# Performance work log

Measured on AMD Instinct MI355X. Metric: run time of the kernel, lower is better.

## Reference

```python
import jax, jax.numpy as jnp
import numpy as np
import math

D = 2048
NH = 16
HD = D // NH
MULT = 4
EPS = 1e-6


def rmsnorm(x, g):
    norm = jax.lax.rsqrt(jnp.mean(x * x, axis=-1, keepdims=True) + EPS)
    return g * x * norm


def setup_inputs() -> dict:
    key = jax.random.key(0)
    ks = jax.random.split(key, 8)
    s = 0.02  # keep activations in a sane range
    return {
        "x": jax.random.normal(ks[0], (2, 2048, D), dtype=jnp.float32),
        "g1": jnp.ones((D,), dtype=jnp.float32),
        "wq": jax.random.normal(ks[1], (D, D), dtype=jnp.float32) * s,
        "wk": jax.random.normal(ks[2], (D, D), dtype=jnp.float32) * s,
        "wv": jax.random.normal(ks[3], (D, D), dtype=jnp.float32) * s,
        "wo": jax.random.normal(ks[4], (D, D), dtype=jnp.float32) * s,
        "g2": jnp.ones((D,), dtype=jnp.float32),
        "w_up": jax.random.normal(ks[5], (2 * D * MULT, D), dtype=jnp.float32) * s,
        "w_down": jax.random.normal(ks[6], (D, D * MULT), dtype=jnp.float32) * s,
    }


def reference(x, g1, wq, wk, wv, wo, g2, w_up, w_down):
    B, T, _ = x.shape
    # --- causal self-attention with pre-RMSNorm ---
    h = rmsnorm(x, g1)
    q = (h @ wq.T).reshape(B, T, NH, HD).transpose(0, 2, 1, 3)  # [B,H,T,hd]
    k = (h @ wk.T).reshape(B, T, NH, HD).transpose(0, 2, 1, 3)
    v = (h @ wv.T).reshape(B, T, NH, HD).transpose(0, 2, 1, 3)
    att = jnp.einsum("bhtd,bhsd->bhts", q, k) / math.sqrt(HD)  # [B,H,T,T]
    neg = jnp.finfo(att.dtype).min
    causal = jnp.triu(jnp.full((T, T), neg, dtype=att.dtype), k=1)
    att = att + causal
    w = jax.nn.softmax(att, axis=-1)
    z = jnp.einsum("bhts,bhsd->bhtd", w, v)  # [B,H,T,hd]
    z = z.transpose(0, 2, 1, 3).reshape(B, T, D)
    x = x + z @ wo.T
    # --- SwiGLU-style FFN (GELU gate) with pre-RMSNorm ---
    h2 = rmsnorm(x, g2)
    uv = h2 @ w_up.T  # [B,T,2*D*MULT]
    u, vgate = jnp.split(uv, 2, axis=-1)
    ff = (jax.nn.gelu(u, approximate=False) * vgate) @ w_down.T
    return x + ff
```

## Files before the change

### kernel.cpp

```cpp
#include <hip/hip_runtime.h>
#include <math.h>

typedef __bf16 bf16_t;
typedef __bf16 bf16x8 __attribute__((ext_vector_type(8)));
typedef __bf16 bf16x4 __attribute__((ext_vector_type(4)));
typedef float f32x4 __attribute__((ext_vector_type(4)));

#define D_MODEL 2048
#define N_HEADS 16
#define HEAD_D 128
#define SEQ 2048
#define NTOK 4096
#define DFF 8192
#define UPN 16384

#define GLDS16(g, l) __builtin_amdgcn_global_load_lds( \
    (const __attribute__((address_space(1))) void*)(g), \
    (__attribute__((address_space(3))) void*)(l), 16, 0, 0)

__global__ __launch_bounds__(256) void cvt_bf16_kernel(const float* __restrict__ in,
                                                       bf16_t* __restrict__ out, long n4) {
    long i = (long)blockIdx.x * 256 + threadIdx.x;
    long stride = (long)gridDim.x * 256;
    for (; i < n4; i += stride) {
        float4 f = ((const float4*)in)[i];
        bf16x4 v;
        v[0] = (bf16_t)f.x; v[1] = (bf16_t)f.y; v[2] = (bf16_t)f.z; v[3] = (bf16_t)f.w;
        ((bf16x4*)out)[i] = v;
    }
}

__global__ __launch_bounds__(256) void rmsnorm_kernel(const float* __restrict__ x,
                                                      const float* __restrict__ g,
                                                      bf16_t* __restrict__ out) {
    int row = blockIdx.x;
    const float* xr = x + (size_t)row * D_MODEL;
    int c0 = threadIdx.x * 8;
    float4 a = *(const float4*)&xr[c0];
    float4 b = *(const float4*)&xr[c0 + 4];
    float ss = a.x*a.x + a.y*a.y + a.z*a.z + a.w*a.w
             + b.x*b.x + b.y*b.y + b.z*b.z + b.w*b.w;
    #pragma unroll
    for (int off = 1; off < 64; off <<= 1) ss += __shfl_xor(ss, off);
    __shared__ float red[4];
    if ((threadIdx.x & 63) == 0) red[threadIdx.x >> 6] = ss;
    __syncthreads();
    float norm = rsqrtf((red[0] + red[1] + red[2] + red[3]) * (1.f / D_MODEL) + 1e-6f);
    float4 ga = *(const float4*)&g[c0];
    float4 gb = *(const float4*)&g[c0 + 4];
    bf16x8 o;
    o[0] = (bf16_t)(a.x * ga.x * norm); o[1] = (bf16_t)(a.y * ga.y * norm);
    o[2] = (bf16_t)(a.z * ga.z * norm); o[3] = (bf16_t)(a.w * ga.w * norm);
    o[4] = (bf16_t)(b.x * gb.x * norm); o[5] = (bf16_t)(b.y * gb.y * norm);
    o[6] = (bf16_t)(b.z * gb.z * norm); o[7] = (bf16_t)(b.w * gb.w * norm);
    *(bf16x8*)&out[(size_t)row * D_MODEL + c0] = o;
}

template<int EPI>
__global__ __launch_bounds__(256)
void gemm_bt(const bf16_t* __restrict__ A, const bf16_t* __restrict__ W,
             void* __restrict__ outp, const float* __restrict__ res,
             int M, int N, int K, float alpha)
{
    __shared__ __align__(16) bf16_t As[128 * 32];
    __shared__ __align__(16) bf16_t Bs[128 * 32];
    const int tid = threadIdx.x;
    const int m0 = blockIdx.y * 128, n0 = blockIdx.x * 128;
    const int wave = tid >> 6, lane = tid & 63;
    const int wr = wave >> 1, wc = wave & 1;
    const int lr = lane & 15, lg = lane >> 4;
    const int srow = (lane >> 2), scol = (lane & 3) * 8;
    f32x4 acc[4][4] = {};
    for (int k0 = 0; k0 < K; k0 += 32) {
        __syncthreads();
        #pragma unroll
        for (int t = 0; t < 2; ++t) {
            int rbase = wave * 32 + t * 16;
            int r = rbase + srow;
            GLDS16(&A[(size_t)(m0 + r) * K + k0 + scol], &As[rbase * 32]);
            GLDS16(&W[(size_t)(n0 + r) * K + k0 + scol], &Bs[rbase * 32]);
        }
        __syncthreads();
        bf16x8 af[4], bfr[4];
        #pragma unroll
        for (int m = 0; m < 4; ++m) af[m] = *(const bf16x8*)&As[(wr * 64 + m * 16 + lr) * 32 + lg * 8];
        #pragma unroll
        for (int n = 0; n < 4; ++n) bfr[n] = *(const bf16x8*)&Bs[(wc * 64 + n * 16 + lr) * 32 + lg * 8];
        #pragma unroll
        for (int m = 0; m < 4; ++m)
            #pragma unroll
            for (int n = 0; n < 4; ++n)
                acc[m][n] = __builtin_amdgcn_mfma_f32_16x16x32_bf16(af[m], bfr[n], acc[m][n], 0, 0, 0);
    }
    #pragma unroll
    for (int m = 0; m < 4; ++m)
        #pragma unroll
        for (int n = 0; n < 4; ++n) {
            int row = m0 + wr * 64 + m * 16 + lg * 4;
            int col = n0 + wc * 64 + n * 16 + lr;
            #pragma unroll
            for (int r = 0; r < 4; ++r) {
                float v = acc[m][n][r];
                if (EPI == 0) {
                    ((bf16_t*)outp)[(size_t)(row + r) * N + col] = (bf16_t)(v * alpha);
                } else if (EPI == 1) {
                    size_t idx = (size_t)(row + r) * N + col;
                    ((float*)outp)[idx] = res[idx] + v;
                } else {
                    int gr = row + r;
                    size_t idx = ((size_t)((gr >> 11) * 16 + (col >> 7)) * 128 + (col & 127)) * 2048
                               + (gr & 2047);
                    ((bf16_t*)outp)[idx] = (bf16_t)v;
                }
            }
        }
}

__global__ __launch_bounds__(256)
void gemm_upgate(const bf16_t* __restrict__ A, const bf16_t* __restrict__ W,
                 bf16_t* __restrict__ act)
{
    __shared__ __align__(16) bf16_t As[128 * 32];
    __shared__ __align__(16) bf16_t Bu[64 * 32];
    __shared__ __align__(16) bf16_t Bv[64 * 32];
    const int tid = threadIdx.x;
    const int m0 = blockIdx.y * 128, n0 = blockIdx.x * 64;
    const int wave = tid >> 6, lane = tid & 63;
    const int wr = wave >> 1, wc = wave & 1;
    const int lr = lane & 15, lg = lane >> 4;
    const int srow = (lane >> 2), scol = (lane & 3) * 8;
    f32x4 accu[4][2] = {}, accv[4][2] = {};
    for (int k0 = 0; k0 < D_MODEL; k0 += 32) {
        __syncthreads();
        #pragma unroll
        for (int t = 0; t < 2; ++t) {
            int rbase = wave * 32 + t * 16;
            GLDS16(&A[(size_t)(m0 + rbase + srow) * D_MODEL + k0 + scol], &As[rbase * 32]);
        }
        {
            int rbase = wave * 16;
            GLDS16(&W[(size_t)(n0 + rbase + srow) * D_MODEL + k0 + scol], &Bu[rbase * 32]);
            GLDS16(&W[(size_t)(DFF + n0 + rbase + srow) * D_MODEL + k0 + scol], &Bv[rbase * 32]);
        }
        __syncthreads();
        bf16x8 af[4], bu[2], bv[2];
        #pragma unroll
        for (int m = 0; m < 4; ++m) af[m] = *(const bf16x8*)&As[(wr * 64 + m * 16 + lr) * 32 + lg * 8];
        #pragma unroll
        for (int n = 0; n < 2; ++n) {
            bu[n] = *(const bf16x8*)&Bu[(wc * 32 + n * 16 + lr) * 32 + lg * 8];
            bv[n] = *(const bf16x8*)&Bv[(wc * 32 + n * 16 + lr) * 32 + lg * 8];
        }
        #pragma unroll
        for (int m = 0; m < 4; ++m)
            #pragma unroll
            for (int n = 0; n < 2; ++n) {
                accu[m][n] = __builtin_amdgcn_mfma_f32_16x16x32_bf16(af[m], bu[n], accu[m][n], 0, 0, 0);
                accv[m][n] = __builtin_amdgcn_mfma_f32_16x16x32_bf16(af[m], bv[n], accv[m][n], 0, 0, 0);
            }
    }
    #pragma unroll
    for (int m = 0; m < 4; ++m)
        #pragma unroll
        for (int n = 0; n < 2; ++n)
            #pragma unroll
            for (int r = 0; r < 4; ++r) {
                int row = m0 + wr * 64 + m * 16 + lg * 4 + r;
                int col = n0 + wc * 32 + n * 16 + lr;
                float u = accu[m][n][r], vg = accv[m][n][r];
                float ge = 0.5f * u * (1.f + erff(u * 0.70710678118654752f));
                act[(size_t)row * DFF + col] = (bf16_t)(ge * vg);
            }
}

__global__ __launch_bounds__(256)
void attn_kernel(const bf16_t* __restrict__ Q, const bf16_t* __restrict__ K,
                 const bf16_t* __restrict__ Vt, bf16_t* __restrict__ Z)
{
    const int qt = gridDim.x - 1 - blockIdx.x;
    const int h = blockIdx.y, b = blockIdx.z;
    const int q0 = qt * 64;
    const int tid = threadIdx.x, wave = tid >> 6, lane = tid & 63;
    const int lr = lane & 15, lg = lane >> 4;

    __shared__ __align__(16) bf16_t Qs[64 * 136];
    __shared__ __align__(16) bf16_t Ks[64 * 136];
    __shared__ __align__(16) bf16_t Vts[128 * 72];
    __shared__ __align__(16) bf16_t Ps[4][16 * 72];

    const size_t base = ((size_t)b * SEQ) * D_MODEL + (size_t)h * HEAD_D;
    const size_t vbase = (size_t)(b * N_HEADS + h) * HEAD_D * SEQ;

    #pragma unroll
    for (int i = 0; i < 4; ++i) {
        int v = tid + 256 * i;
        int row = v >> 4, cv = (v & 15) * 8;
        *(uint4*)&Qs[row * 136 + cv] = *(const uint4*)&Q[base + (size_t)(q0 + row) * D_MODEL + cv];
    }

    f32x4 o[8] = {};
    float mrun[4], lrun[4];
    #pragma unroll
    for (int r = 0; r < 4; ++r) { mrun[r] = -1e30f; lrun[r] = 0.f; }

    for (int kt = 0; kt <= qt; ++kt) {
        const int k0 = kt * 64;
        __syncthreads();
        #pragma unroll
        for (int i = 0; i < 4; ++i) {
            int v = tid + 256 * i;
            int row = v >> 4, cv = (v & 15) * 8;
            *(uint4*)&Ks[row * 136 + cv] = *(const uint4*)&K[base + (size_t)(k0 + row) * D_MODEL + cv];
            int d = v >> 3, c8 = (v & 7) * 8;
            *(uint4*)&Vts[d * 72 + c8] = *(const uint4*)&Vt[vbase + (size_t)d * SEQ + k0 + c8];
        }
        __syncthreads();

        f32x4 s[4] = {};
        #pragma unroll
        for (int kk = 0; kk < 4; ++kk) {
            bf16x8 aq = *(const bf16x8*)&Qs[(wave * 16 + lr) * 136 + kk * 32 + lg * 8];
            #pragma unroll
            for (int nb = 0; nb < 4; ++nb) {
                bf16x8 bk = *(const bf16x8*)&Ks[(nb * 16 + lr) * 136 + kk * 32 + lg * 8];
                s[nb] = __builtin_amdgcn_mfma_f32_16x16x32_bf16(aq, bk, s[nb], 0, 0, 0);
            }
        }
        if (kt == qt) {
            #pragma unroll
            for (int nb = 0; nb < 4; ++nb)
                #pragma unroll
                for (int r = 0; r < 4; ++r) {
                    int qrel = 16 * wave + lg * 4 + r;
                    int krel = nb * 16 + lr;
                    if (krel > qrel) s[nb][r] = -1e30f;
                }
        }
        float resc[4];
        #pragma unroll
        for (int r = 0; r < 4; ++r) {
            float mx = fmaxf(fmaxf(s[0][r], s[1][r]), fmaxf(s[2][r], s[3][r]));
            #pragma unroll
            for (int off = 1; off < 16; off <<= 1) mx = fmaxf(mx, __shfl_xor(mx, off));
            float mnew = fmaxf(mrun[r], mx);
            resc[r] = __expf(mrun[r] - mnew);
            float sum = 0.f;
            #pragma unroll
            for (int nb = 0; nb < 4; ++nb) {
                float p = __expf(s[nb][r] - mnew);
                s[nb][r] = p;
                sum += p;
            }
            #pragma unroll
            for (int off = 1; off < 16; off <<= 1) sum += __shfl_xor(sum, off);
            lrun[r] = lrun[r] * resc[r] + sum;
            mrun[r] = mnew;
        }
        #pragma unroll
        for (int ob = 0; ob < 8; ++ob)
            #pragma unroll
            for (int r = 0; r < 4; ++r) o[ob][r] *= resc[r];
        #pragma unroll
        for (int nb = 0; nb < 4; ++nb)
            #pragma unroll
            for (int r = 0; r < 4; ++r)
                Ps[wave][(lg * 4 + r) * 72 + nb * 16 + lr] = (bf16_t)s[nb][r];
        #pragma unroll
        for (int kk = 0; kk < 2; ++kk) {
            bf16x8 ap = *(const bf16x8*)&Ps[wave][lr * 72 + kk * 32 + lg * 8];
            #pragma unroll
            for (int ob = 0; ob < 8; ++ob) {
                bf16x8 bv = *(const bf16x8*)&Vts[(ob * 16 + lr) * 72 + kk * 32 + lg * 8];
                o[ob] = __builtin_amdgcn_mfma_f32_16x16x32_bf16(ap, bv, o[ob], 0, 0, 0);
            }
        }
    }
    #pragma unroll
    for (int ob = 0; ob < 8; ++ob)
        #pragma unroll
        for (int r = 0; r < 4; ++r) {
            int t = q0 + 16 * wave + lg * 4 + r;
            Z[base + (size_t)t * D_MODEL + ob * 16 + lr] = (bf16_t)(o[ob][r] / lrun[r]);
        }
}

extern "C" void kernel_launch(void* const* d_in, const int* in_sizes, int n_in,
                              void* d_out, int out_size, void* d_ws, size_t ws_size,
                              hipStream_t stream)
{
    const float* x   = (const float*)d_in[0];
    const float* g1  = (const float*)d_in[1];
    const float* wq  = (const float*)d_in[2];
    const float* wk  = (const float*)d_in[3];
    const float* wv  = (const float*)d_in[4];
    const float* wo  = (const float*)d_in[5];
    const float* g2  = (const float*)d_in[6];
    const float* wup = (const float*)d_in[7];
    const float* wdn = (const float*)d_in[8];
    float* out = (float*)d_out;

    char* wsp = (char*)d_ws;
    size_t off = 0;
    auto alloc = [&](size_t bytes) { void* p = wsp + off; off += (bytes + 255) & ~255ull; return p; };
    bf16_t* wq_b  = (bf16_t*)alloc((size_t)D_MODEL * D_MODEL * 2);
    bf16_t* wk_b  = (bf16_t*)alloc((size_t)D_MODEL * D_MODEL * 2);
    bf16_t* wv_b  = (bf16_t*)alloc((size_t)D_MODEL * D_MODEL * 2);
    bf16_t* wo_b  = (bf16_t*)alloc((size_t)D_MODEL * D_MODEL * 2);
    bf16_t* wup_b = (bf16_t*)alloc((size_t)UPN * D_MODEL * 2);
    bf16_t* wdn_b = (bf16_t*)alloc((size_t)D_MODEL * DFF * 2);
    bf16_t* h_b   = (bf16_t*)alloc((size_t)NTOK * D_MODEL * 2);
    bf16_t* q_b   = (bf16_t*)alloc((size_t)NTOK * D_MODEL * 2);
    bf16_t* k_b   = (bf16_t*)alloc((size_t)NTOK * D_MODEL * 2);
    bf16_t* vt_b  = (bf16_t*)alloc((size_t)NTOK * D_MODEL * 2);
    bf16_t* z_b   = (bf16_t*)alloc((size_t)NTOK * D_MODEL * 2);
    float*  x1    = (float*) alloc((size_t)NTOK * D_MODEL * 4);
    bf16_t* h2_b  = (bf16_t*)alloc((size_t)NTOK * D_MODEL * 2);
    bf16_t* act_b = (bf16_t*)alloc((size_t)NTOK * DFF * 2);

    auto cvt = [&](const float* in, bf16_t* outb, long n) {
        long n4 = n / 4;
        long nb = (n4 + 255) / 256;
        int blocks = nb > 2048 ? 2048 : (int)nb;
        cvt_bf16_kernel<<<blocks, 256, 0, stream>>>(in, outb, n4);
    };
    cvt(wq,  wq_b,  (long)D_MODEL * D_MODEL);
    cvt(wk,  wk_b,  (long)D_MODEL * D_MODEL);
    cvt(wv,  wv_b,  (long)D_MODEL * D_MODEL);
    cvt(wo,  wo_b,  (long)D_MODEL * D_MODEL);
    cvt(wup, wup_b, (long)UPN * D_MODEL);
    cvt(wdn, wdn_b, (long)D_MODEL * DFF);

    rmsnorm_kernel<<<NTOK, 256, 0, stream>>>(x, g1, h_b);

    dim3 g_qkv(D_MODEL / 128, NTOK / 128);
    gemm_bt<0><<<g_qkv, 256, 0, stream>>>(h_b, wq_b, q_b, nullptr, NTOK, D_MODEL, D_MODEL, 0.08838834764831845f);
    gemm_bt<0><<<g_qkv, 256, 0, stream>>>(h_b, wk_b, k_b, nullptr, NTOK, D_MODEL, D_MODEL, 1.0f);
    gemm_bt<2><<<g_qkv, 256, 0, stream>>>(h_b, wv_b, vt_b, nullptr, NTOK, D_MODEL, D_MODEL, 1.0f);

    attn_kernel<<<dim3(SEQ / 64, N_HEADS, 2), 256, 0, stream>>>(q_b, k_b, vt_b, z_b);

    gemm_bt<1><<<g_qkv, 256, 0, stream>>>(z_b, wo_b, x1, x, NTOK, D_MODEL, D_MODEL, 1.0f);

    rmsnorm_kernel<<<NTOK, 256, 0, stream>>>(x1, g2, h2_b);

    gemm_upgate<<<dim3(DFF / 64, NTOK / 128), 256, 0, stream>>>(h2_b, wup_b, act_b);

    gemm_bt<1><<<dim3(D_MODEL / 128, NTOK / 128), 256, 0, stream>>>(act_b, wdn_b, out, x1, NTOK, D_MODEL, DFF, 1.0f);
}
```

Before: 1.075 ms.

## Replace GEMMs with double-buffered 256x128 swizzled MFMA kernel and fuse QKV

All projection GEMMs now run through one templated 512-thread kernel. It uses 256x128 output tiles and a K step of 64, with double-buffered LDS filled by global_load_lds and explicit vmcnt waits. LDS uses an XOR swizzle to avoid bank conflicts, and a block-id remap spreads neighbouring tiles across XCDs. The Q, K and V projections are merged into a single launch over a 6144-column weight, with per-column-range epilogues that include the transposed V write. The intent is more data reuse and less load/compute serialisation. The cost is heavy LDS use (up to 128KB per block) and a reliance on the three QKV weight buffers sitting contiguously in memory.

After: 1.023 ms. 4.8% less time.

```diff
diff --git a/kernel.cpp b/kernel.cpp
--- a/kernel.cpp
+++ b/kernel.cpp
@@ -56,121 +56,190 @@
     *(bf16x8*)&out[(size_t)row * D_MODEL + c0] = o;
 }
 
-template<int EPI>
-__global__ __launch_bounds__(256)
-void gemm_bt(const bf16_t* __restrict__ A, const bf16_t* __restrict__ W,
-             void* __restrict__ outp, const float* __restrict__ res,
-             int M, int N, int K, float alpha)
+__device__ __forceinline__ void stage_half(const bf16_t* gbase, int ldK,
+                                           bf16_t* lds_half, int wave, int lane) {
+    #pragma unroll
+    for (int i = 0; i < 2; ++i) {
+        int rl = i * 64 + wave * 8 + (lane >> 3);
+        int cb = ((lane & 7) ^ (lane >> 3)) << 4;
+        const char* src = (const char*)(gbase + (size_t)rl * ldK) + cb;
+        char* dst = (char*)lds_half + i * 8192 + wave * 1024;
+        GLDS16(src, dst);
+    }
+}
+
+template<int MODE>
+__global__ __launch_bounds__(512)
+void gemm8(const bf16_t* __restrict__ A, const bf16_t* __restrict__ W,
+           void* __restrict__ o0, void* __restrict__ o1, void* __restrict__ o2,
+           const float* __restrict__ res, int nbx, int K)
 {
-    __shared__ __align__(16) bf16_t As[128 * 32];
-    __shared__ __align__(16) bf16_t Bs[128 * 32];
+    __shared__ __align__(16) bf16_t As[2][256 * 64];
+    __shared__ __align__(16) bf16_t Bs[2][(MODE == 2 ? 2 : 1) * 128 * 64];
+
     const int tid = threadIdx.x;
-    const int m0 = blockIdx.y * 128, n0 = blockIdx.x * 128;
     const int wave = tid >> 6, lane = tid & 63;
-    const int wr = wave >> 1, wc = wave & 1;
     const int lr = lane & 15, lg = lane >> 4;
-    const int srow = (lane >> 2), scol = (lane & 3) * 8;
-    f32x4 acc[4][4] = {};
-    for (int k0 = 0; k0 < K; k0 += 32) {
-        __syncthreads();
-        #pragma unroll
-        for (int t = 0; t < 2; ++t) {
-            int rbase = wave * 32 + t * 16;
-            int r = rbase + srow;
-            GLDS16(&A[(size_t)(m0 + r) * K + k0 + scol], &As[rbase * 32]);
-            GLDS16(&W[(size_t)(n0 + r) * K + k0 + scol], &Bs[rbase * 32]);
-        }
-        __syncthreads();
-        bf16x8 af[4], bfr[4];
-        #pragma unroll
-        for (int m = 0; m < 4; ++m) af[m] = *(const bf16x8*)&As[(wr * 64 + m * 16 + lr) * 32 + lg * 8];
-        #pragma unroll
-        for (int n = 0; n < 4; ++n) bfr[n] = *(const bf16x8*)&Bs[(wc * 64 + n * 16 + lr) * 32 + lg * 8];
-        #pragma unroll
-        for (int m = 0; m < 4; ++m)
-            #pragma unroll
-            for (int n = 0; n < 4; ++n)
-                acc[m][n] = __builtin_amdgcn_mfma_f32_16x16x32_bf16(af[m], bfr[n], acc[m][n], 0, 0, 0);
-    }
-    #pragma unroll
-    for (int m = 0; m < 4; ++m)
-        #pragma unroll
-        for (int n = 0; n < 4; ++n) {
-            int row = m0 + wr * 64 + m * 16 + lg * 4;
-            int col = n0 + wc * 64 + n * 16 + lr;
-            #pragma unroll
-            for (int r = 0; r < 4; ++r) {
-                float v = acc[m][n][r];
-                if (EPI == 0) {
-                    ((bf16_t*)outp)[(size_t)(row + r) * N + col] = (bf16_t)(v * alpha);
-                } else if (EPI == 1) {
-                    size_t idx = (size_t)(row + r) * N + col;
-                    ((float*)outp)[idx] = res[idx] + v;
+    const int wm = wave >> 1, wn = wave & 1;
+
+    const int nwg = gridDim.x, bid = blockIdx.x;
+    const int cpx = nwg >> 3;
+    const int s = (bid & 7) * cpx + (bid >> 3);
+    const int bx = s % nbx, by = s / nbx;
+    const int bm0 = by * 256, bn0 = bx * 128;
+
+    const bf16_t* Asrc0 = A + (size_t)bm0 * K;
+    const bf16_t* Asrc1 = A + (size_t)(bm0 + 128) * K;
+    const bf16_t* Bsrc0 = W + (size_t)bn0 * K;
+    const bf16_t* Bsrc1 = (MODE == 2) ? (W + (size_t)(DFF + bn0) * K) : nullptr;
+
+    auto issue = [&](int t) {
+        int p = t & 1;
+        size_t k0 = (size_t)t * 64;
+        stage_half(Asrc0 + k0, K, &As[p][0], wave, lane);
+        stage_half(Asrc1 + k0, K, &As[p][128 * 64], wave, lane);
+        stage_half(Bsrc0 + k0, K, &Bs[p][0], wave, lane);
+        if constexpr (MODE == 2)
+            stage_half(Bsrc1 + k0, K, &Bs[p][128 * 64], wave, lane);
+    };
+
+    f32x4 accu[4][4] = {};
+    f32x4 accv[4][4] = {};
+
+    const int NKT = K >> 6;
+    issue(0);
+    for (int j = 0; j < NKT; ++j) {
+        if (j + 1 < NKT) {
+            issue(j + 1);
+            if constexpr (MODE == 2) asm volatile("s_waitcnt vmcnt(8)" ::: "memory");
+            else                     asm volatile("s_waitcnt vmcnt(6)" ::: "memory");
+        } else {
+            asm volatile("s_waitcnt vmcnt(0)" ::: "memory");
+        }
+        __builtin_amdgcn_s_barrier();
+
+        const bf16_t* Ap = &As[j & 1][0];
+        const bf16_t* Bp = &Bs[j & 1][0];
+
+        bf16x8 af[4][2];
+        #pragma unroll
+        for (int m = 0; m < 4; ++m) {
+            int row = wm * 64 + m * 16 + lr;
+            #pragma unroll
+            for (int kk = 0; kk < 2; ++kk)
+                af[m][kk] = *(const bf16x8*)&Ap[row * 64 + ((kk * 32 + lg * 8) ^ ((row & 7) << 3))];
+        }
+
+        #pragma unroll
+        for (int qn = 0; qn < 2; ++qn) {
+            if constexpr (MODE != 2) {
+                bf16x8 bfr[2][2];
+                #pragma unroll
+                for (int n2 = 0; n2 < 2; ++n2) {
+                    int brow = wn * 64 + (qn * 2 + n2) * 16 + lr;
+                    #pragma unroll
+                    for (int kk = 0; kk < 2; ++kk)
+                        bfr[n2][kk] = *(const bf16x8*)&Bp[brow * 64 + ((kk * 32 + lg * 8) ^ ((brow & 7) << 3))];
+                }
+                __builtin_amdgcn_s_setprio(1);
+                #pragma unroll
+                for (int m = 0; m < 4; ++m)
+                    #pragma unroll
+                    for (int n2 = 0; n2 < 2; ++n2)
+                        #pragma unroll
+                        for (int kk = 0; kk < 2; ++kk)
+                            accu[m][qn * 2 + n2] = __builtin_amdgcn_mfma_f32_16x16x32_bf16(
+                                af[m][kk], bfr[n2][kk], accu[m][qn * 2 + n2], 0, 0, 0);
+                __builtin_amdgcn_s_setprio(0);
+                __builtin_amdgcn_s_barrier();
+            } else {
+                #pragma unroll
+                for (int qv = 0; qv < 2; ++qv) {
+                    const bf16_t* Bpq = Bp + qv * (128 * 64);
+                    bf16x8 bfr[2][2];
+                    #pragma unroll
+                    for (int n2 = 0; n2 < 2; ++n2) {
+                        int brow = wn * 64 + (qn * 2 + n2) * 16 + lr;
+                        #pragma unroll
+                        for (int kk = 0; kk < 2; ++kk)
+                            bfr[n2][kk] = *(const bf16x8*)&Bpq[brow * 64 + ((kk * 32 + lg * 8) ^ ((brow & 7) << 3))];
+                    }
+                    f32x4 (*accp)[4] = qv ? accv : accu;
+                    __builtin_amdgcn_s_setprio(1);
+                    #pragma unroll
+                    for (int m = 0; m < 4; ++m)
+                        #pragma unroll
+                        for (int n2 = 0; n2 < 2; ++n2)
+                            #pragma unroll
+                            for (int kk = 0; kk < 2; ++kk)
+                                accp[m][qn * 2 + n2] = __builtin_amdgcn_mfma_f32_16x16x32_bf16(
+                                    af[m][kk], bfr[n2][kk], accp[m][qn * 2 + n2], 0, 0, 0);
+                    __builtin_amdgcn_s_setprio(0);
+                    __builtin_amdgcn_s_barrier();
+                }
+            }
+        }
+    }
+
+    const int r0 = lg * 4;
+    if constexpr (MODE == 0) {
+        const float qs = 0.08838834764831845f;
+        const int th = bn0 >> 11;
+        #pragma unroll
+        for (int m = 0; m < 4; ++m) {
+            int grow = bm0 + wm * 64 + m * 16 + r0;
+            #pragma unroll
+            for (int n = 0; n < 4; ++n) {
+                int gcol = bn0 + wn * 64 + n * 16 + lr;
+                int c = gcol & 2047;
+                if (th == 0) {
+                    #pragma unroll
+                    for (int r = 0; r < 4; ++r)
+                        ((bf16_t*)o0)[(size_t)(grow + r) * D_MODEL + c] = (bf16_t)(accu[m][n][r] * qs);
+                } else if (th == 1) {
+                    #pragma unroll
+                    for (int r = 0; r < 4; ++r)
+                        ((bf16_t*)o1)[(size_t)(grow + r) * D_MODEL + c] = (bf16_t)accu[m][n][r];
                 } else {
-                    int gr = row + r;
-                    size_t idx = ((size_t)((gr >> 11) * 16 + (col >> 7)) * 128 + (col & 127)) * 2048
-                               + (gr & 2047);
-                    ((bf16_t*)outp)[idx] = (bf16_t)v;
-                }
-            }
-        }
-}
-
-__global__ __launch_bounds__(256)
-void gemm_upgate(const bf16_t* __restrict__ A, const bf16_t* __restrict__ W,
-                 bf16_t* __restrict__ act)
-{
-    __shared__ __align__(16) bf16_t As[128 * 32];
-    __shared__ __align__(16) bf16_t Bu[64 * 32];
-    __shared__ __align__(16) bf16_t Bv[64 * 32];
-    const int tid = threadIdx.x;
-    const int m0 = blockIdx.y * 128, n0 = blockIdx.x * 64;
-    const int wave = tid >> 6, lane = tid & 63;
-    const int wr = wave >> 1, wc = wave & 1;
-    const int lr = lane & 15, lg = lane >> 4;
-    const int srow = (lane >> 2), scol = (lane & 3) * 8;
-    f32x4 accu[4][2] = {}, accv[4][2] = {};
-    for (int k0 = 0; k0 < D_MODEL; k0 += 32) {
-        __syncthreads();
-        #pragma unroll
-        for (int t = 0; t < 2; ++t) {
-            int rbase = wave * 32 + t * 16;
-            GLDS16(&A[(size_t)(m0 + rbase + srow) * D_MODEL + k0 + scol], &As[rbase * 32]);
-        }
-        {
-            int rbase = wave * 16;
-            GLDS16(&W[(size_t)(n0 + rbase + srow) * D_MODEL + k0 + scol], &Bu[rbase * 32]);
-            GLDS16(&W[(size_t)(DFF + n0 + rbase + srow) * D_MODEL + k0 + scol], &Bv[rbase * 32]);
-        }
-        __syncthreads();
-        bf16x8 af[4], bu[2], bv[2];
-        #pragma unroll
-        for (int m = 0; m < 4; ++m) af[m] = *(const bf16x8*)&As[(wr * 64 + m * 16 + lr) * 32 + lg * 8];
-        #pragma unroll
-        for (int n = 0; n < 2; ++n) {
-            bu[n] = *(const bf16x8*)&Bu[(wc * 32 + n * 16 + lr) * 32 + lg * 8];
-            bv[n] = *(const bf16x8*)&Bv[(wc * 32 + n * 16 + lr) * 32 + lg * 8];
-        }
-        #pragma unroll
-        for (int m = 0; m < 4; ++m)
-            #pragma unroll
-            for (int n = 0; n < 2; ++n) {
-                accu[m][n] = __builtin_amdgcn_mfma_f32_16x16x32_bf16(af[m], bu[n], accu[m][n], 0, 0, 0);
-                accv[m][n] = __builtin_amdgcn_mfma_f32_16x16x32_bf16(af[m], bv[n], accv[m][n], 0, 0, 0);
-            }
-    }
-    #pragma unroll
-    for (int m = 0; m < 4; ++m)
-        #pragma unroll
-        for (int n = 0; n < 2; ++n)
-            #pragma unroll
-            for (int r = 0; r < 4; ++r) {
-                int row = m0 + wr * 64 + m * 16 + lg * 4 + r;
-                int col = n0 + wc * 32 + n * 16 + lr;
-                float u = accu[m][n][r], vg = accv[m][n][r];
-                float ge = 0.5f * u * (1.f + erff(u * 0.70710678118654752f));
-                act[(size_t)row * DFF + col] = (bf16_t)(ge * vg);
-            }
+                    int hh = c >> 7, d = c & 127;
+                    int bb = grow >> 11, t0 = grow & 2047;
+                    bf16x4 st;
+                    #pragma unroll
+                    for (int r = 0; r < 4; ++r) st[r] = (bf16_t)accu[m][n][r];
+                    *(bf16x4*)&((bf16_t*)o2)[((size_t)(bb * N_HEADS + hh) * HEAD_D + d) * SEQ + t0] = st;
+                }
+            }
+        }
+    } else if constexpr (MODE == 1) {
+        #pragma unroll
+        for (int m = 0; m < 4; ++m) {
+            int grow = bm0 + wm * 64 + m * 16 + r0;
+            #pragma unroll
+            for (int n = 0; n < 4; ++n) {
+                int gcol = bn0 + wn * 64 + n * 16 + lr;
+                #pragma unroll
+                for (int r = 0; r < 4; ++r) {
+                    size_t idx = (size_t)(grow + r) * D_MODEL + gcol;
+                    ((float*)o0)[idx] = res[idx] + accu[m][n][r];
+                }
+            }
+        }
+    } else {
+        #pragma unroll
+        for (int m = 0; m < 4; ++m) {
+            int grow = bm0 + wm * 64 + m * 16 + r0;
+            #pragma unroll
+            for (int n = 0; n < 4; ++n) {
+                int gcol = bn0 + wn * 64 + n * 16 + lr;
+                #pragma unroll
+                for (int r = 0; r < 4; ++r) {
+                    float u = accu[m][n][r], vg = accv[m][n][r];
+                    float ge = 0.5f * u * (1.f + erff(u * 0.70710678118654752f));
+                    ((bf16_t*)o0)[(size_t)(grow + r) * DFF + gcol] = (bf16_t)(ge * vg);
+                }
+            }
+        }
+    }
 }
 
 __global__ __launch_bounds__(256)
@@ -332,18 +401,15 @@
 
     rmsnorm_kernel<<<NTOK, 256, 0, stream>>>(x, g1, h_b);
 
-    dim3 g_qkv(D_MODEL / 128, NTOK / 128);
-    gemm_bt<0><<<g_qkv, 256, 0, stream>>>(h_b, wq_b, q_b, nullptr, NTOK, D_MODEL, D_MODEL, 0.08838834764831845f);
-    gemm_bt<0><<<g_qkv, 256, 0, stream>>>(h_b, wk_b, k_b, nullptr, NTOK, D_MODEL, D_MODEL, 1.0f);
-    gemm_bt<2><<<g_qkv, 256, 0, stream>>>(h_b, wv_b, vt_b, nullptr, NTOK, D_MODEL, D_MODEL, 1.0f);
+    gemm8<0><<<48 * 16, 512, 0, stream>>>(h_b, wq_b, q_b, k_b, vt_b, nullptr, 48, D_MODEL);
 
     attn_kernel<<<dim3(SEQ / 64, N_HEADS, 2), 256, 0, stream>>>(q_b, k_b, vt_b, z_b);
 
-    gemm_bt<1><<<g_qkv, 256, 0, stream>>>(z_b, wo_b, x1, x, NTOK, D_MODEL, D_MODEL, 1.0f);
+    gemm8<1><<<16 * 16, 512, 0, stream>>>(z_b, wo_b, x1, nullptr, nullptr, x, 16, D_MODEL);
 
     rmsnorm_kernel<<<NTOK, 256, 0, stream>>>(x1, g2, h2_b);
 
-    gemm_upgate<<<dim3(DFF / 64, NTOK / 128), 256, 0, stream>>>(h2_b, wup_b, act_b);
-
-    gemm_bt<1><<<dim3(D_MODEL / 128, NTOK / 128), 256, 0, stream>>>(act_b, wdn_b, out, x1, NTOK, D_MODEL, DFF, 1.0f);
-}
+    gemm8<2><<<64 * 16, 512, 0, stream>>>(h2_b, wup_b, act_b, nullptr, nullptr, nullptr, 64, D_MODEL);
+
+    gemm8<1><<<16 * 16, 512, 0, stream>>>(act_b, wdn_b, out, nullptr, nullptr, x1, 16, DFF);
+}
```
